# Kernel optimization log

Hardware: AMD Instinct MI355X
Metric: run time of the kernel (lower is better)

The kernel has to match this reference:

```python
import jax, jax.numpy as jnp
import numpy as np

N, IN_DIM, POS_DIM, HID, HEADS, OUT = 8192, 128, 16, 128, 4, 40
HD = HID // HEADS


def setup_inputs() -> dict:
    key = jax.random.key(0)
    ks = jax.random.split(key, 12)
    w = lambda k, shape: (jax.random.normal(k, shape, jnp.float32) * 0.05)
    return {
        "x": jax.random.normal(ks[0], (N, IN_DIM), jnp.float32),
        "pos_enc": jax.random.normal(ks[1], (N, POS_DIM), jnp.float32),  # unused in forward (faithful)
        "dense_sp_matrix": jax.random.randint(ks[2], (N, N), 0, 11).astype(jnp.float32),
        "W_in": w(ks[3], (HID, IN_DIM)),
        "b_in": jnp.zeros((HID,), jnp.float32),
        "in_proj_w": w(ks[4], (3 * HID, HID)),
        "in_proj_b": jnp.zeros((3 * HID,), jnp.float32),
        "out_proj_w": w(ks[5], (HID, HID)),
        "out_proj_b": jnp.zeros((HID,), jnp.float32),
        "W_out": w(ks[6], (OUT, HID)),
        "b_out": jnp.zeros((OUT,), jnp.float32),
        "attn_bias_scale": jnp.array([10.0], jnp.float32),
    }


def reference(x, pos_enc, dense_sp_matrix, W_in, b_in, in_proj_w, in_proj_b,
              out_proj_w, out_proj_b, W_out, b_out, attn_bias_scale):
    # input projection
    h = x @ W_in.T + b_in  # [N, HID]
    # attn bias: distance d -> scale/d ; d==0 -> 0 ; nan/inf in sp -> -scale
    sp = jnp.nan_to_num(dense_sp_matrix, nan=-1.0, posinf=-1.0, neginf=-1.0)
    bias = attn_bias_scale[0] * jnp.nan_to_num(1.0 / sp, nan=0.0, posinf=0.0, neginf=0.0)  # [N, N]
    # single MHA layer (eval mode: attention dropout and residual dropout are identity)
    qkv = h @ in_proj_w.T + in_proj_b  # [N, 3*HID]
    q, k, v = jnp.split(qkv, 3, axis=-1)
    q = q.reshape(N, HEADS, HD).transpose(1, 0, 2)  # [H, N, hd]
    k = k.reshape(N, HEADS, HD).transpose(1, 0, 2)
    v = v.reshape(N, HEADS, HD).transpose(1, 0, 2)
    scores = jnp.einsum("hnd,hmd->hnm", q, k) / np.sqrt(HD).astype(np.float32) + bias[None]  # [H, N, N]
    attn = jax.nn.softmax(scores, axis=-1)
    o = jnp.einsum("hnm,hmd->hnd", attn, v).transpose(1, 0, 2).reshape(N, HID)
    o = o @ out_proj_w.T + out_proj_b
    h = h + jax.nn.relu(o)  # residual
    logits = h @ W_out.T + b_out  # [N, OUT]
    return jax.nn.log_softmax(logits, axis=-1)
```

## Files before the change

### kernel.cpp

```cpp
#include <hip/hip_runtime.h>
#include <hip/hip_bf16.h>
#include <hip/hip_runtime_api.h>

#define NROWS 8192
#define HID 128
#define OUTC 40

typedef unsigned short ushort_t;
typedef __attribute__((ext_vector_type(8))) short bf16x8;
typedef __attribute__((ext_vector_type(4))) short short4v;
typedef __attribute__((ext_vector_type(4))) float f32x4;

__device__ __forceinline__ short f2bf(float f) {
    unsigned int u = __float_as_uint(f);
    unsigned int r = (u + 0x7FFFu + ((u >> 16) & 1u)) >> 16;
    return (short)r;
}
__device__ __forceinline__ float bf2f(ushort_t b) {
    return __uint_as_float(((unsigned int)b) << 16);
}
__device__ __forceinline__ float exp2_fast(float x) {
#if __has_builtin(__builtin_amdgcn_exp2f)
    return __builtin_amdgcn_exp2f(x);
#else
    return exp2f(x);
#endif
}
__device__ __forceinline__ float bias_of16(float f, float scale2) {
    float r = scale2 * __builtin_amdgcn_rcpf(f);
    bool bad = (__float_as_uint(r) & 0x7F800000u) == 0x7F800000u;
    return bad ? -16.f : r - 16.f;
}


__global__ __launch_bounds__(256) void k_prep(const float* __restrict__ x,
                                              const float* __restrict__ Wi,
                                              const float* __restrict__ Wp,
                                              const float* __restrict__ Wo,
                                              const float* __restrict__ Wout,
                                              ushort_t* __restrict__ xfr,
                                              ushort_t* __restrict__ wifr,
                                              ushort_t* __restrict__ wpfr,
                                              ushort_t* __restrict__ wofr,
                                              ushort_t* __restrict__ woutfr) {
    int rb = blockIdx.x;
    const float* src; ushort_t* dst; int rt; int nrows;
    if (rb < 512)      { src = x;    dst = xfr;    rt = rb;       nrows = 1 << 30; }
    else if (rb < 520) { src = Wi;   dst = wifr;   rt = rb - 512; nrows = 1 << 30; }
    else if (rb < 544) { src = Wp;   dst = wpfr;   rt = rb - 520; nrows = 1 << 30; }
    else if (rb < 552) { src = Wo;   dst = wofr;   rt = rb - 544; nrows = 1 << 30; }
    else               { src = Wout; dst = woutfr; rt = rb - 552; nrows = OUTC; }
    int t = threadIdx.x;
    int r = t >> 4, c8 = t & 15;
    int row = rt * 16 + r;
    float4 a = {0.f, 0.f, 0.f, 0.f}, b = {0.f, 0.f, 0.f, 0.f};
    if (row < nrows) {
        a = *(const float4*)(src + (size_t)row * 128 + c8 * 8);
        b = *(const float4*)(src + (size_t)row * 128 + c8 * 8 + 4);
    }
    short4v s0 = {f2bf(a.x), f2bf(a.y), f2bf(a.z), f2bf(a.w)};
    short4v s1 = {f2bf(b.x), f2bf(b.y), f2bf(b.z), f2bf(b.w)};
    ushort_t* d = dst + ((((size_t)rt * 4 + (c8 >> 2)) * 4 + (c8 & 3)) * 16 + r) * 8;
    *(short4v*)d = s0;
    *(short4v*)(d + 4) = s1;
}

__global__ __launch_bounds__(256) void k_qkv_fused(const ushort_t* __restrict__ xfr,
                                                   const ushort_t* __restrict__ wifr,
                                                   const float* __restrict__ bi,
                                                   const ushort_t* __restrict__ wpfr,
                                                   const float* __restrict__ bp,
                                                   ushort_t* __restrict__ hbf,
                                                   ushort_t* __restrict__ qfr,
                                                   ushort_t* __restrict__ kfr,
                                                   ushort_t* __restrict__ vfr) {
    __shared__ __align__(16) ushort_t h_s[16][136];
    const int w = threadIdx.x >> 6, lane = threadIdx.x & 63;
    const int l15 = lane & 15, quad = lane >> 4;
    const int rt = blockIdx.x;
    const int r0 = rt * 16;

    {
        bf16x8 af[4], bfr[2][4];
#pragma unroll
        for (int kf = 0; kf < 4; ++kf)
            af[kf] = *(const bf16x8*)(xfr + (((size_t)rt * 4 + kf) * 4 + quad) * 128 + l15 * 8);
#pragma unroll
        for (int nt = 0; nt < 2; ++nt)
#pragma unroll
            for (int kf = 0; kf < 4; ++kf)
                bfr[nt][kf] = *(const bf16x8*)(wifr + (((size_t)(w * 2 + nt) * 4 + kf) * 4 + quad) * 128 + l15 * 8);
#pragma unroll
        for (int nt = 0; nt < 2; ++nt) {
            float bias = bi[w * 32 + nt * 16 + l15];
            f32x4 c = {bias, bias, bias, bias};
#pragma unroll
            for (int kf = 0; kf < 4; ++kf)
                c = __builtin_amdgcn_mfma_f32_16x16x32_bf16(af[kf], bfr[nt][kf], c, 0, 0, 0);
            int col = w * 32 + nt * 16 + l15;
#pragma unroll
            for (int r = 0; r < 4; ++r) {
                int row = quad * 4 + r;
                short hv = f2bf(c[r]);
                h_s[row][col] = (ushort_t)hv;
                hbf[(size_t)(r0 + row) * 128 + col] = (ushort_t)hv;
            }
        }
    }
    __syncthreads();
    bf16x8 af2[4];
#pragma unroll
    for (int kf = 0; kf < 4; ++kf)
        af2[kf] = *(const bf16x8*)&h_s[l15][kf * 32 + quad * 8];
    const float QS = 0.25503482459918643f;
#pragma unroll
    for (int nt = 0; nt < 6; ++nt) {
        const int n0 = w * 96 + nt * 16;
        bf16x8 bfr[4];
#pragma unroll
        for (int kf = 0; kf < 4; ++kf)
            bfr[kf] = *(const bf16x8*)(wpfr + (((size_t)(w * 6 + nt) * 4 + kf) * 4 + quad) * 128 + l15 * 8);
        float bias = bp[n0 + l15];
        f32x4 c = {bias, bias, bias, bias};
#pragma unroll
        for (int kf = 0; kf < 4; ++kf)
            c = __builtin_amdgcn_mfma_f32_16x16x32_bf16(af2[kf], bfr[kf], c, 0, 0, 0);
        if (n0 < 256) {
            int col = (n0 < 128) ? (n0 + l15) : (n0 - 128 + l15);
            ushort_t* dstf = (n0 < 128) ? qfr : kfr;
            float sc = (n0 < 128) ? QS : 1.0f;
            int hh = col >> 5, qd = (col >> 3) & 3, j = col & 7;
#pragma unroll
            for (int r = 0; r < 4; ++r) {
                int token = r0 + quad * 4 + r;
                dstf[((((size_t)(token >> 4) * 4 + hh) * 4 + qd) * 16 + (token & 15)) * 8 + j] =
                    (ushort_t)f2bf(c[r] * sc);
            }
        } else {
            int d = n0 - 256 + l15;
            int hh = d >> 5, dt = (d >> 4) & 1, dl = d & 15;
            int key0 = r0 + quad * 4;
            int kb = key0 >> 5, qk = (key0 >> 3) & 3, j0 = key0 & 7;
            short4v pk = {f2bf(c[0]), f2bf(c[1]), f2bf(c[2]), f2bf(c[3])};
            *(short4v*)&vfr[(((((size_t)kb * 4 + hh) * 2 + dt) * 4 + qk) * 16 + dl) * 8 + j0] = pk;
        }
    }
}

__global__ __launch_bounds__(256, 4) void k_attn(const ushort_t* __restrict__ qfr,
                                                 const ushort_t* __restrict__ kfr,
                                                 const ushort_t* __restrict__ vfr,
                                                 const float* __restrict__ sp,
                                                 const float* __restrict__ scale_p,
                                                 ushort_t* __restrict__ pob,
                                                 float* __restrict__ pml) {
    __shared__ __align__(16) float bias_s[2][32][68];
    __shared__ __align__(16) ushort_t p_s[4][2][16][72];

    const int t = threadIdx.x;
    const int h = t >> 6;
    const int lane = t & 63, l15 = lane & 15, quad = lane >> 4;
    const int qt = blockIdx.x & 255;
    const int quarter = blockIdx.x >> 8;
    const int q0 = qt * 32;
    const int k0 = quarter * 2048;
    const float scale2 = scale_p[0] * 1.4426950408889634f;

    const int brow = t >> 3, bc8 = (t & 7) * 8;
    const float* spb = sp + (size_t)(q0 + brow) * NROWS + k0 + bc8;

    bf16x8 bq[2];
#pragma unroll
    for (int qq = 0; qq < 2; ++qq)
        bq[qq] = *(const bf16x8*)(qfr + ((((size_t)(q0 >> 4) + qq) * 4 + h) * 4 + quad) * 128 + l15 * 8);

    bf16x8 af[4], vf[2][2];
#pragma unroll
    for (int c = 0; c < 4; ++c)
        af[c] = *(const bf16x8*)(kfr + ((((size_t)(k0 >> 4) + c) * 4 + h) * 4 + quad) * 128 + l15 * 8);
#pragma unroll
    for (int dt = 0; dt < 2; ++dt)
#pragma unroll
        for (int kc = 0; kc < 2; ++kc)
            vf[dt][kc] = *(const bf16x8*)(vfr + (((((size_t)(k0 >> 5) + kc) * 4 + h) * 2 + dt) * 4 + quad) * 128 + l15 * 8);

    {
        float4 a = *(const float4*)spb;
        float4 b = *(const float4*)(spb + 4);
        f32x4 ca = {bias_of16(a.x, scale2), bias_of16(a.y, scale2), bias_of16(a.z, scale2), bias_of16(a.w, scale2)};
        f32x4 cb = {bias_of16(b.x, scale2), bias_of16(b.y, scale2), bias_of16(b.z, scale2), bias_of16(b.w, scale2)};
        *(f32x4*)&bias_s[0][brow][bc8] = ca;
        *(f32x4*)&bias_s[0][brow][bc8 + 4] = cb;
    }
    float4 brg[2][2];
    brg[0][0] = *(const float4*)(spb + 64);
    brg[0][1] = *(const float4*)(spb + 68);
    brg[1][0] = *(const float4*)(spb + 128);
    brg[1][1] = *(const float4*)(spb + 132);
    __syncthreads();

    f32x4 oacc[2][2] = {};
    float l[2] = {0.f, 0.f};

    for (int it = 0; it < 32; ++it) {
        const int cur = it & 1;
        f32x4 sacc[4][2];
#pragma unroll
        for (int c = 0; c < 4; ++c)
#pragma unroll
            for (int qq = 0; qq < 2; ++qq)
                sacc[c][qq] = *(const f32x4*)&bias_s[cur][qq * 16 + l15][c * 16 + quad * 4];
#pragma unroll
        for (int c = 0; c < 4; ++c)
#pragma unroll
            for (int qq = 0; qq < 2; ++qq)
                sacc[c][qq] = __builtin_amdgcn_mfma_f32_16x16x32_bf16(af[c], bq[qq], sacc[c][qq], 0, 0, 0);
        if (it < 31) {
            size_t rtk = (size_t)(k0 >> 4) + (it + 1) * 4;
#pragma unroll
            for (int c = 0; c < 4; ++c)
                af[c] = *(const bf16x8*)(kfr + (((rtk + c) * 4 + h) * 4 + quad) * 128 + l15 * 8);
        }
#pragma unroll
        for (int qq = 0; qq < 2; ++qq) {
            float lsum = 0.f;
#pragma unroll
            for (int c = 0; c < 4; ++c)
#pragma unroll
                for (int r = 0; r < 4; ++r) {
                    float p = exp2_fast(sacc[c][qq][r]);
                    sacc[c][qq][r] = p;
                    lsum += p;
                }
            l[qq] += lsum;
        }
#pragma unroll
        for (int qq = 0; qq < 2; ++qq)
#pragma unroll
            for (int c = 0; c < 4; ++c) {
                unsigned b0 = __float_as_uint(sacc[c][qq][0]);
                unsigned b1 = __float_as_uint(sacc[c][qq][1]);
                unsigned b2 = __float_as_uint(sacc[c][qq][2]);
                unsigned b3 = __float_as_uint(sacc[c][qq][3]);
                uint2 pw;
                pw.x = __builtin_amdgcn_perm(b1, b0, 0x07060302);
                pw.y = __builtin_amdgcn_perm(b3, b2, 0x07060302);
                *(uint2*)&p_s[h][qq][l15][c * 16 + quad * 4] = pw;
            }
        asm volatile("s_waitcnt lgkmcnt(0)" ::: "memory");
        bf16x8 pf[2][2];
#pragma unroll
        for (int qq = 0; qq < 2; ++qq)
#pragma unroll
            for (int kc = 0; kc < 2; ++kc)
                pf[qq][kc] = *(const bf16x8*)&p_s[h][qq][l15][kc * 32 + quad * 8];
#pragma unroll
        for (int dt = 0; dt < 2; ++dt)
#pragma unroll
            for (int qq = 0; qq < 2; ++qq) {
                oacc[dt][qq] = __builtin_amdgcn_mfma_f32_16x16x32_bf16(vf[dt][0], pf[qq][0], oacc[dt][qq], 0, 0, 0);
                oacc[dt][qq] = __builtin_amdgcn_mfma_f32_16x16x32_bf16(vf[dt][1], pf[qq][1], oacc[dt][qq], 0, 0, 0);
            }
        if (it < 31) {
            size_t kb = (size_t)(k0 >> 5) + (it + 1) * 2;
#pragma unroll
            for (int dt = 0; dt < 2; ++dt)
#pragma unroll
                for (int kc = 0; kc < 2; ++kc)
                    vf[dt][kc] = *(const bf16x8*)(vfr + ((((kb + kc) * 4 + h) * 2 + dt) * 4 + quad) * 128 + l15 * 8);
        }
        if (it < 31) {
            f32x4 ca = {bias_of16(brg[cur][0].x, scale2), bias_of16(brg[cur][0].y, scale2),
                        bias_of16(brg[cur][0].z, scale2), bias_of16(brg[cur][0].w, scale2)};
            f32x4 cb = {bias_of16(brg[cur][1].x, scale2), bias_of16(brg[cur][1].y, scale2),
                        bias_of16(brg[cur][1].z, scale2), bias_of16(brg[cur][1].w, scale2)};
            *(f32x4*)&bias_s[1 - cur][brow][bc8] = ca;
            *(f32x4*)&bias_s[1 - cur][brow][bc8 + 4] = cb;
            if (it < 29) {
                brg[cur][0] = *(const float4*)(spb + (it + 3) * 64);
                brg[cur][1] = *(const float4*)(spb + (it + 3) * 64 + 4);
            }
        }
        __syncthreads();
    }

#pragma unroll
    for (int qq = 0; qq < 2; ++qq) {
        float lt = l[qq];
        lt += __shfl_xor(lt, 16, 64);
        lt += __shfl_xor(lt, 32, 64);
        int qtile = qt * 2 + qq;
        if (quad == 0)
            pml[((size_t)(q0 + qq * 16 + l15) * 4 + h) * 4 + quarter] = lt;
#pragma unroll
        for (int dt = 0; dt < 2; ++dt) {
            short4v pk = {f2bf(oacc[dt][qq][0]), f2bf(oacc[dt][qq][1]),
                          f2bf(oacc[dt][qq][2]), f2bf(oacc[dt][qq][3])};
            *(short4v*)&pob[(((((size_t)qtile * 4 + h) * 4 + quarter) * 2 + dt) * 256)
                            + quad * 64 + l15 * 4] = pk;
        }
    }
}

__global__ __launch_bounds__(256) void k_epi(const ushort_t* __restrict__ hbf,
                                             const ushort_t* __restrict__ pob,
                                             const float* __restrict__ pml,
                                             const ushort_t* __restrict__ wofr,
                                             const float* __restrict__ bo,
                                             const ushort_t* __restrict__ woutfr,
                                             const float* __restrict__ bout,
                                             float* __restrict__ out) {
    __shared__ __align__(16) ushort_t hr_s[16][136];
    const int w = threadIdx.x >> 6, lane = threadIdx.x & 63;
    const int l15 = lane & 15, quad = lane >> 4;
    const int rt = blockIdx.x;
    const int r0 = rt * 16;

    {
        bf16x8 af[4], bfr[2][4];
#pragma unroll
        for (int kf = 0; kf < 4; ++kf) {
            float4 lv = *(const float4*)(pml + ((size_t)(r0 + l15) * 4 + kf) * 4);
            float linv = 1.f / (lv.x + lv.y + lv.z + lv.w);
            float acc[8] = {0.f, 0.f, 0.f, 0.f, 0.f, 0.f, 0.f, 0.f};
#pragma unroll
            for (int j = 0; j < 4; ++j) {
                size_t base = ((((size_t)rt * 4 + kf) * 4 + j) * 2 + (quad >> 1)) * 256
                              + (quad & 1) * 128 + l15 * 4;
                short4v v0 = *(const short4v*)(pob + base);
                short4v v1 = *(const short4v*)(pob + base + 64);
#pragma unroll
                for (int e = 0; e < 4; ++e) {
                    acc[e] += bf2f((ushort_t)v0[e]);
                    acc[4 + e] += bf2f((ushort_t)v1[e]);
                }
            }
            bf16x8 a;
#pragma unroll
            for (int e = 0; e < 8; ++e) a[e] = f2bf(acc[e] * linv);
            af[kf] = a;
        }
#pragma unroll
        for (int nt = 0; nt < 2; ++nt)
#pragma unroll
            for (int kf = 0; kf < 4; ++kf)
                bfr[nt][kf] = *(const bf16x8*)(wofr + (((size_t)(w * 2 + nt) * 4 + kf) * 4 + quad) * 128 + l15 * 8);
#pragma unroll
        for (int nt = 0; nt < 2; ++nt) {
            float bias = bo[w * 32 + nt * 16 + l15];
            f32x4 c = {bias, bias, bias, bias};
#pragma unroll
            for (int kf = 0; kf < 4; ++kf)
                c = __builtin_amdgcn_mfma_f32_16x16x32_bf16(af[kf], bfr[nt][kf], c, 0, 0, 0);
            int col = w * 32 + nt * 16 + l15;
#pragma unroll
            for (int r = 0; r < 4; ++r) {
                int row = quad * 4 + r;
                float val = fmaxf(c[r], 0.f) + bf2f(hbf[(size_t)(r0 + row) * 128 + col]);
                hr_s[row][col] = (ushort_t)f2bf(val);
            }
        }
    }
    __syncthreads();
    if (w == 0) {
        f32x4 c[3];
#pragma unroll
        for (int mt = 0; mt < 3; ++mt)
#pragma unroll
            for (int r = 0; r < 4; ++r) {
                int oc = mt * 16 + quad * 4 + r;
                c[mt][r] = (oc < OUTC) ? bout[oc] : 0.f;
            }
#pragma unroll
        for (int kf = 0; kf < 4; ++kf) {
            bf16x8 bfrag = *(const bf16x8*)&hr_s[l15][kf * 32 + quad * 8];
#pragma unroll
            for (int mt = 0; mt < 3; ++mt) {
                bf16x8 afr = *(const bf16x8*)(woutfr + (((size_t)mt * 4 + kf) * 4 + quad) * 128 + l15 * 8);
                c[mt] = __builtin_amdgcn_mfma_f32_16x16x32_bf16(afr, bfrag, c[mt], 0, 0, 0);
            }
        }
        float mx = -1e30f;
#pragma unroll
        for (int mt = 0; mt < 3; ++mt)
#pragma unroll
            for (int r = 0; r < 4; ++r) {
                int oc = mt * 16 + quad * 4 + r;
                if (oc >= OUTC) c[mt][r] = -1e30f;
                mx = fmaxf(mx, c[mt][r]);
            }
        mx = fmaxf(mx, __shfl_xor(mx, 16, 64));
        mx = fmaxf(mx, __shfl_xor(mx, 32, 64));
        float ssum = 0.f;
#pragma unroll
        for (int mt = 0; mt < 3; ++mt)
#pragma unroll
            for (int r = 0; r < 4; ++r) ssum += __expf(c[mt][r] - mx);
        ssum += __shfl_xor(ssum, 16, 64);
        ssum += __shfl_xor(ssum, 32, 64);
        float lse = __logf(ssum) + mx;
        int row = r0 + l15;
#pragma unroll
        for (int mt = 0; mt < 2; ++mt) {
            float4 st = make_float4(c[mt][0] - lse, c[mt][1] - lse, c[mt][2] - lse, c[mt][3] - lse);
            *(float4*)(out + (size_t)row * OUTC + mt * 16 + quad * 4) = st;
        }
        if (quad < 2) {
            float4 st = make_float4(c[2][0] - lse, c[2][1] - lse, c[2][2] - lse, c[2][3] - lse);
            *(float4*)(out + (size_t)row * OUTC + 32 + quad * 4) = st;
        }
    }
}

extern "C" void kernel_launch(void* const* d_in, const int* in_sizes, int n_in,
                              void* d_out, int out_size, void* d_ws, size_t ws_size,
                              hipStream_t stream) {
    const float* x          = (const float*)d_in[0];
    const float* sp         = (const float*)d_in[2];
    const float* W_in       = (const float*)d_in[3];
    const float* b_in       = (const float*)d_in[4];
    const float* in_proj_w  = (const float*)d_in[5];
    const float* in_proj_b  = (const float*)d_in[6];
    const float* out_proj_w = (const float*)d_in[7];
    const float* out_proj_b = (const float*)d_in[8];
    const float* W_out      = (const float*)d_in[9];
    const float* b_out      = (const float*)d_in[10];
    const float* scale      = (const float*)d_in[11];

    float*    pml    = (float*)d_ws;
    ushort_t* pob    = (ushort_t*)(pml + (size_t)NROWS * 16);
    ushort_t* xfr    = pob + (size_t)NROWS * 512;
    ushort_t* qfr    = xfr + (size_t)NROWS * 128;
    ushort_t* kfr    = qfr + (size_t)NROWS * 128;
    ushort_t* vfr    = kfr + (size_t)NROWS * 128;
    ushort_t* hbf    = vfr + (size_t)NROWS * 128;
    ushort_t* wifr   = hbf + (size_t)NROWS * 128;
    ushort_t* wpfr   = wifr + 128 * 128;
    ushort_t* wofr   = wpfr + 384 * 128;
    ushort_t* woutfr = wofr + 128 * 128;
    float*    out    = (float*)d_out;

    hipLaunchKernelGGL(k_prep, dim3(555), dim3(256), 0, stream,
                       x, W_in, in_proj_w, out_proj_w, W_out, xfr, wifr, wpfr, wofr, woutfr);
    hipLaunchKernelGGL(k_qkv_fused, dim3(NROWS / 16), dim3(256), 0, stream,
                       xfr, wifr, b_in, wpfr, in_proj_b, hbf, qfr, kfr, vfr);
    hipLaunchKernelGGL(k_attn, dim3(256 * 4), dim3(256), 0, stream,
                       qfr, kfr, vfr, sp, scale, pob, pml);
    hipLaunchKernelGGL(k_epi, dim3(NROWS / 16), dim3(256), 0, stream,
                       hbf, pob, pml, wofr, out_proj_b, woutfr, b_out, out);
}
```

Measured before the change: 520.2 us.

## Split keys into halves and stage bias in larger batched rounds

The attention kernel now splits the key range into two halves instead of four, halving the grid and the partial-output/partial-sum workspace that the epilogue reduces. Bias from the dense distance matrix is loaded in 256-column rounds using nontemporal loads into a larger single LDS buffer. That cuts block-wide barriers from one per 64-key step to two per 256 keys. The cost is fewer blocks (512 on a 256-CU part), more registers held for the prefetch with launch bounds lowered to 2, and less latency hiding, since the bias write waits behind a barrier instead of being double-buffered.

```diff
diff --git a/kernel.cpp b/kernel.cpp
--- a/kernel.cpp
+++ b/kernel.cpp
@@ -147,27 +147,27 @@
     }
 }
 
-__global__ __launch_bounds__(256, 4) void k_attn(const ushort_t* __restrict__ qfr,
+__global__ __launch_bounds__(256, 2) void k_attn(const ushort_t* __restrict__ qfr,
                                                  const ushort_t* __restrict__ kfr,
                                                  const ushort_t* __restrict__ vfr,
                                                  const float* __restrict__ sp,
                                                  const float* __restrict__ scale_p,
                                                  ushort_t* __restrict__ pob,
                                                  float* __restrict__ pml) {
-    __shared__ __align__(16) float bias_s[2][32][68];
+    __shared__ __align__(16) float bias_s[32][260];
     __shared__ __align__(16) ushort_t p_s[4][2][16][72];
 
     const int t = threadIdx.x;
     const int h = t >> 6;
     const int lane = t & 63, l15 = lane & 15, quad = lane >> 4;
     const int qt = blockIdx.x & 255;
-    const int quarter = blockIdx.x >> 8;
+    const int half = blockIdx.x >> 8;
     const int q0 = qt * 32;
-    const int k0 = quarter * 2048;
+    const int k0 = half * 4096;
     const float scale2 = scale_p[0] * 1.4426950408889634f;
 
-    const int brow = t >> 3, bc8 = (t & 7) * 8;
-    const float* spb = sp + (size_t)(q0 + brow) * NROWS + k0 + bc8;
+    const int brow = t >> 3, bcol = (t & 7) * 4;
+    const float* spb = sp + (size_t)(q0 + brow) * NROWS + k0 + bcol;
 
     bf16x8 bq[2];
 #pragma unroll
@@ -184,104 +184,106 @@
         for (int kc = 0; kc < 2; ++kc)
             vf[dt][kc] = *(const bf16x8*)(vfr + (((((size_t)(k0 >> 5) + kc) * 4 + h) * 2 + dt) * 4 + quad) * 128 + l15 * 8);
 
-    {
-        float4 a = *(const float4*)spb;
-        float4 b = *(const float4*)(spb + 4);
-        f32x4 ca = {bias_of16(a.x, scale2), bias_of16(a.y, scale2), bias_of16(a.z, scale2), bias_of16(a.w, scale2)};
-        f32x4 cb = {bias_of16(b.x, scale2), bias_of16(b.y, scale2), bias_of16(b.z, scale2), bias_of16(b.w, scale2)};
-        *(f32x4*)&bias_s[0][brow][bc8] = ca;
-        *(f32x4*)&bias_s[0][brow][bc8 + 4] = cb;
-    }
-    float4 brg[2][2];
-    brg[0][0] = *(const float4*)(spb + 64);
-    brg[0][1] = *(const float4*)(spb + 68);
-    brg[1][0] = *(const float4*)(spb + 128);
-    brg[1][1] = *(const float4*)(spb + 132);
+    f32x4 breg[8];
+#pragma unroll
+    for (int k = 0; k < 8; ++k)
+        breg[k] = __builtin_nontemporal_load((const f32x4*)(spb + k * 32));
+#pragma unroll
+    for (int k = 0; k < 8; ++k) {
+        f32x4 cv = {bias_of16(breg[k][0], scale2), bias_of16(breg[k][1], scale2),
+                    bias_of16(breg[k][2], scale2), bias_of16(breg[k][3], scale2)};
+        *(f32x4*)&bias_s[brow][k * 32 + bcol] = cv;
+    }
     __syncthreads();
 
     f32x4 oacc[2][2] = {};
     float l[2] = {0.f, 0.f};
 
-    for (int it = 0; it < 32; ++it) {
-        const int cur = it & 1;
-        f32x4 sacc[4][2];
-#pragma unroll
-        for (int c = 0; c < 4; ++c)
+    for (int rnd = 0; rnd < 16; ++rnd) {
+        if (rnd < 15) {
+#pragma unroll
+            for (int k = 0; k < 8; ++k)
+                breg[k] = __builtin_nontemporal_load((const f32x4*)(spb + (rnd + 1) * 256 + k * 32));
+        }
+#pragma unroll
+        for (int j = 0; j < 4; ++j) {
+            const int it = rnd * 4 + j;
+            f32x4 sacc[4][2];
+#pragma unroll
+            for (int c = 0; c < 4; ++c)
+#pragma unroll
+                for (int qq = 0; qq < 2; ++qq)
+                    sacc[c][qq] = *(const f32x4*)&bias_s[qq * 16 + l15][j * 64 + c * 16 + quad * 4];
+#pragma unroll
+            for (int c = 0; c < 4; ++c)
+#pragma unroll
+                for (int qq = 0; qq < 2; ++qq)
+                    sacc[c][qq] = __builtin_amdgcn_mfma_f32_16x16x32_bf16(af[c], bq[qq], sacc[c][qq], 0, 0, 0);
+            if (it < 63) {
+                size_t rtk = (size_t)(k0 >> 4) + (it + 1) * 4;
+#pragma unroll
+                for (int c = 0; c < 4; ++c)
+                    af[c] = *(const bf16x8*)(kfr + (((rtk + c) * 4 + h) * 4 + quad) * 128 + l15 * 8);
+            }
+#pragma unroll
+            for (int qq = 0; qq < 2; ++qq) {
+                float lsum = 0.f;
+#pragma unroll
+                for (int c = 0; c < 4; ++c)
+#pragma unroll
+                    for (int r = 0; r < 4; ++r) {
+                        float p = exp2_fast(sacc[c][qq][r]);
+                        sacc[c][qq][r] = p;
+                        lsum += p;
+                    }
+                l[qq] += lsum;
+            }
 #pragma unroll
             for (int qq = 0; qq < 2; ++qq)
-                sacc[c][qq] = *(const f32x4*)&bias_s[cur][qq * 16 + l15][c * 16 + quad * 4];
-#pragma unroll
-        for (int c = 0; c < 4; ++c)
+#pragma unroll
+                for (int c = 0; c < 4; ++c) {
+                    unsigned b0 = __float_as_uint(sacc[c][qq][0]);
+                    unsigned b1 = __float_as_uint(sacc[c][qq][1]);
+                    unsigned b2 = __float_as_uint(sacc[c][qq][2]);
+                    unsigned b3 = __float_as_uint(sacc[c][qq][3]);
+                    uint2 pw;
+                    pw.x = __builtin_amdgcn_perm(b1, b0, 0x07060302);
+                    pw.y = __builtin_amdgcn_perm(b3, b2, 0x07060302);
+                    *(uint2*)&p_s[h][qq][l15][c * 16 + quad * 4] = pw;
+                }
+            asm volatile("s_waitcnt lgkmcnt(0)" ::: "memory");
+            bf16x8 pf[2][2];
 #pragma unroll
             for (int qq = 0; qq < 2; ++qq)
-                sacc[c][qq] = __builtin_amdgcn_mfma_f32_16x16x32_bf16(af[c], bq[qq], sacc[c][qq], 0, 0, 0);
-        if (it < 31) {
-            size_t rtk = (size_t)(k0 >> 4) + (it + 1) * 4;
-#pragma unroll
-            for (int c = 0; c < 4; ++c)
-                af[c] = *(const bf16x8*)(kfr + (((rtk + c) * 4 + h) * 4 + quad) * 128 + l15 * 8);
-        }
-#pragma unroll
-        for (int qq = 0; qq < 2; ++qq) {
-            float lsum = 0.f;
-#pragma unroll
-            for (int c = 0; c < 4; ++c)
-#pragma unroll
-                for (int r = 0; r < 4; ++r) {
-                    float p = exp2_fast(sacc[c][qq][r]);
-                    sacc[c][qq][r] = p;
-                    lsum += p;
+#pragma unroll
+                for (int kc = 0; kc < 2; ++kc)
+                    pf[qq][kc] = *(const bf16x8*)&p_s[h][qq][l15][kc * 32 + quad * 8];
+#pragma unroll
+            for (int dt = 0; dt < 2; ++dt)
+#pragma unroll
+                for (int qq = 0; qq < 2; ++qq) {
+                    oacc[dt][qq] = __builtin_amdgcn_mfma_f32_16x16x32_bf16(vf[dt][0], pf[qq][0], oacc[dt][qq], 0, 0, 0);
+                    oacc[dt][qq] = __builtin_amdgcn_mfma_f32_16x16x32_bf16(vf[dt][1], pf[qq][1], oacc[dt][qq], 0, 0, 0);
                 }
-            l[qq] += lsum;
-        }
-#pragma unroll
-        for (int qq = 0; qq < 2; ++qq)
-#pragma unroll
-            for (int c = 0; c < 4; ++c) {
-                unsigned b0 = __float_as_uint(sacc[c][qq][0]);
-                unsigned b1 = __float_as_uint(sacc[c][qq][1]);
-                unsigned b2 = __float_as_uint(sacc[c][qq][2]);
-                unsigned b3 = __float_as_uint(sacc[c][qq][3]);
-                uint2 pw;
-                pw.x = __builtin_amdgcn_perm(b1, b0, 0x07060302);
-                pw.y = __builtin_amdgcn_perm(b3, b2, 0x07060302);
-                *(uint2*)&p_s[h][qq][l15][c * 16 + quad * 4] = pw;
-            }
-        asm volatile("s_waitcnt lgkmcnt(0)" ::: "memory");
-        bf16x8 pf[2][2];
-#pragma unroll
-        for (int qq = 0; qq < 2; ++qq)
-#pragma unroll
-            for (int kc = 0; kc < 2; ++kc)
-                pf[qq][kc] = *(const bf16x8*)&p_s[h][qq][l15][kc * 32 + quad * 8];
-#pragma unroll
-        for (int dt = 0; dt < 2; ++dt)
-#pragma unroll
-            for (int qq = 0; qq < 2; ++qq) {
-                oacc[dt][qq] = __builtin_amdgcn_mfma_f32_16x16x32_bf16(vf[dt][0], pf[qq][0], oacc[dt][qq], 0, 0, 0);
-                oacc[dt][qq] = __builtin_amdgcn_mfma_f32_16x16x32_bf16(vf[dt][1], pf[qq][1], oacc[dt][qq], 0, 0, 0);
-            }
-        if (it < 31) {
-            size_t kb = (size_t)(k0 >> 5) + (it + 1) * 2;
-#pragma unroll
-            for (int dt = 0; dt < 2; ++dt)
-#pragma unroll
-                for (int kc = 0; kc < 2; ++kc)
-                    vf[dt][kc] = *(const bf16x8*)(vfr + ((((kb + kc) * 4 + h) * 2 + dt) * 4 + quad) * 128 + l15 * 8);
-        }
-        if (it < 31) {
-            f32x4 ca = {bias_of16(brg[cur][0].x, scale2), bias_of16(brg[cur][0].y, scale2),
-                        bias_of16(brg[cur][0].z, scale2), bias_of16(brg[cur][0].w, scale2)};
-            f32x4 cb = {bias_of16(brg[cur][1].x, scale2), bias_of16(brg[cur][1].y, scale2),
-                        bias_of16(brg[cur][1].z, scale2), bias_of16(brg[cur][1].w, scale2)};
-            *(f32x4*)&bias_s[1 - cur][brow][bc8] = ca;
-            *(f32x4*)&bias_s[1 - cur][brow][bc8 + 4] = cb;
-            if (it < 29) {
-                brg[cur][0] = *(const float4*)(spb + (it + 3) * 64);
-                brg[cur][1] = *(const float4*)(spb + (it + 3) * 64 + 4);
-            }
-        }
-        __syncthreads();
+            if (it < 63) {
+                size_t kb = (size_t)(k0 >> 5) + (it + 1) * 2;
+#pragma unroll
+                for (int dt = 0; dt < 2; ++dt)
+#pragma unroll
+                    for (int kc = 0; kc < 2; ++kc)
+                        vf[dt][kc] = *(const bf16x8*)(vfr + ((((kb + kc) * 4 + h) * 2 + dt) * 4 + quad) * 128 + l15 * 8);
+            }
+        }
+        if (rnd < 15) {
+            __syncthreads();
+#pragma unroll
+            for (int k = 0; k < 8; ++k) {
+                f32x4 cv = {bias_of16(breg[k][0], scale2), bias_of16(breg[k][1], scale2),
+                            bias_of16(breg[k][2], scale2), bias_of16(breg[k][3], scale2)};
+                *(f32x4*)&bias_s[brow][k * 32 + bcol] = cv;
+            }
+            __syncthreads();
+        }
     }
 
 #pragma unroll
@@ -291,12 +293,12 @@
         lt += __shfl_xor(lt, 32, 64);
         int qtile = qt * 2 + qq;
         if (quad == 0)
-            pml[((size_t)(q0 + qq * 16 + l15) * 4 + h) * 4 + quarter] = lt;
+            pml[((size_t)(q0 + qq * 16 + l15) * 4 + h) * 2 + half] = lt;
 #pragma unroll
         for (int dt = 0; dt < 2; ++dt) {
             short4v pk = {f2bf(oacc[dt][qq][0]), f2bf(oacc[dt][qq][1]),
                           f2bf(oacc[dt][qq][2]), f2bf(oacc[dt][qq][3])};
-            *(short4v*)&pob[(((((size_t)qtile * 4 + h) * 4 + quarter) * 2 + dt) * 256)
+            *(short4v*)&pob[(((((size_t)qtile * 4 + h) * 2 + half) * 2 + dt) * 256)
                             + quad * 64 + l15 * 4] = pk;
         }
     }
@@ -320,12 +322,12 @@
         bf16x8 af[4], bfr[2][4];
 #pragma unroll
         for (int kf = 0; kf < 4; ++kf) {
-            float4 lv = *(const float4*)(pml + ((size_t)(r0 + l15) * 4 + kf) * 4);
-            float linv = 1.f / (lv.x + lv.y + lv.z + lv.w);
+            float2 lv = *(const float2*)(pml + ((size_t)(r0 + l15) * 4 + kf) * 2);
+            float linv = 1.f / (lv.x + lv.y);
             float acc[8] = {0.f, 0.f, 0.f, 0.f, 0.f, 0.f, 0.f, 0.f};
 #pragma unroll
-            for (int j = 0; j < 4; ++j) {
-                size_t base = ((((size_t)rt * 4 + kf) * 4 + j) * 2 + (quad >> 1)) * 256
+            for (int j = 0; j < 2; ++j) {
+                size_t base = ((((size_t)rt * 4 + kf) * 2 + j) * 2 + (quad >> 1)) * 256
                               + (quad & 1) * 128 + l15 * 4;
                 short4v v0 = *(const short4v*)(pob + base);
                 short4v v1 = *(const short4v*)(pob + base + 64);
@@ -428,8 +430,8 @@
     const float* scale      = (const float*)d_in[11];
 
     float*    pml    = (float*)d_ws;
-    ushort_t* pob    = (ushort_t*)(pml + (size_t)NROWS * 16);
-    ushort_t* xfr    = pob + (size_t)NROWS * 512;
+    ushort_t* pob    = (ushort_t*)(pml + (size_t)NROWS * 8);
+    ushort_t* xfr    = pob + (size_t)NROWS * 256;
     ushort_t* qfr    = xfr + (size_t)NROWS * 128;
     ushort_t* kfr    = qfr + (size_t)NROWS * 128;
     ushort_t* vfr    = kfr + (size_t)NROWS * 128;
@@ -444,7 +446,7 @@
                        x, W_in, in_proj_w, out_proj_w, W_out, xfr, wifr, wpfr, wofr, woutfr);
     hipLaunchKernelGGL(k_qkv_fused, dim3(NROWS / 16), dim3(256), 0, stream,
                        xfr, wifr, b_in, wpfr, in_proj_b, hbf, qfr, kfr, vfr);
-    hipLaunchKernelGGL(k_attn, dim3(256 * 4), dim3(256), 0, stream,
+    hipLaunchKernelGGL(k_attn, dim3(256 * 2), dim3(256), 0, stream,
                        qfr, kfr, vfr, sp, scale, pob, pml);
     hipLaunchKernelGGL(k_epi, dim3(NROWS / 16), dim3(256), 0, stream,
                        hbf, pob, pml, wofr, out_proj_b, woutfr, b_out, out);
```

Result: faster. 483.9 us (-7.0%).
